# Optimization experiments

Hardware: AMD Instinct MI355X
Metric: run time of the kernel (lower is better)

The kernel has to match this reference:

```python
import jax, jax.numpy as jnp
import numpy as np

D_MODEL = 1024
N_HEAD = 16
D_HEAD = D_MODEL // N_HEAD


def setup_inputs() -> dict:
    key = jax.random.key(0)
    k_x, k_qkv, k_proj = jax.random.split(key, 3)
    B, T = 2, 2048
    x = jax.random.normal(k_x, (B, T, D_MODEL), dtype=jnp.float32)
    # torch Linear weight [out, in]; y = x @ W.T. Scale ~ kaiming-uniform-ish.
    s = 1.0 / np.sqrt(D_MODEL)
    W_qkv = jax.random.uniform(k_qkv, (3 * D_MODEL, D_MODEL), dtype=jnp.float32, minval=-s, maxval=s)
    W_proj = jax.random.uniform(k_proj, (D_MODEL, D_MODEL), dtype=jnp.float32, minval=-s, maxval=s)
    return {"x": x, "W_qkv": W_qkv, "W_proj": W_proj}


def reference(x, W_qkv, W_proj):
    B, T, C = x.shape
    qkv = jnp.einsum('btc,oc->bto', x, W_qkv)  # [B,T,3C]
    q, k, v = jnp.split(qkv, 3, axis=-1)
    # [B,T,C] -> [B,H,T,Dh]
    def heads(t):
        return t.reshape(B, T, N_HEAD, D_HEAD).transpose(0, 2, 1, 3)
    q, k, v = heads(q), heads(k), heads(v)
    scale = 1.0 / np.sqrt(D_HEAD)
    scores = jnp.einsum('bhqd,bhkd->bhqk', q, k) * scale  # [B,H,T,T]
    causal = jnp.tril(jnp.ones((T, T), dtype=bool))
    scores = jnp.where(causal, scores, jnp.finfo(scores.dtype).min)
    attn = jax.nn.softmax(scores, axis=-1)
    y = jnp.einsum('bhqk,bhkd->bhqd', attn, v)  # [B,H,T,Dh]
    y = y.transpose(0, 2, 1, 3).reshape(B, T, C)
    return jnp.einsum('btc,oc->bto', y, W_proj)
```

## Files before the change

kernel.cpp:

```cpp
#include <hip/hip_runtime.h>

typedef unsigned short u16;
typedef float f32x4 __attribute__((ext_vector_type(4)));
typedef __bf16 bf16x8 __attribute__((ext_vector_type(8)));
typedef unsigned int u32x4 __attribute__((ext_vector_type(4)));
typedef u16 u16x4 __attribute__((ext_vector_type(4)));
typedef u16 u16x8 __attribute__((ext_vector_type(8)));

static __device__ __forceinline__ u16 f2bf(float f) {
  union { __bf16 h; u16 u; } c;
  c.h = (__bf16)f;
  return c.u;
}

static __device__ __forceinline__ void gload_lds16(const void* g, void* l) {
  __builtin_amdgcn_global_load_lds(
      (const __attribute__((address_space(1))) unsigned int*)g,
      (__attribute__((address_space(3))) unsigned int*)l, 16, 0, 0);
}

__global__ __launch_bounds__(256) void cvt3_f32_bf16(const float* __restrict__ a,
                                                     const float* __restrict__ bb,
                                                     const float* __restrict__ cc,
                                                     u16* __restrict__ out,
                                                     int n1, int n2, int n3) {
  int i = blockIdx.x * 256 + threadIdx.x;
  const float* src;
  int j = i;
  if (i < n1) { src = a; }
  else if (i < n1 + n2) { src = bb; j = i - n1; }
  else { src = cc; j = i - n1 - n2; if (j >= n3) return; }
  f32x4 v = *((const f32x4*)src + j);
  u16x4 o;
  o[0] = f2bf(v[0]); o[1] = f2bf(v[1]); o[2] = f2bf(v[2]); o[3] = f2bf(v[3]);
  *((u16x4*)out + i) = o;
}

template<int OUT_BF16>
__global__ __launch_bounds__(256) void gemm_nt(const u16* __restrict__ A,
                                               const u16* __restrict__ B,
                                               void* __restrict__ Cp,
                                               int M, int N, int K, int gy) {
  __shared__ __align__(16) u16 lA[128 * 64];
  __shared__ __align__(16) u16 lB[128 * 64];
  const int tid = threadIdx.x;
  const int lane = tid & 63;
  const int wave = tid >> 6;
  const int wm = wave >> 1, wn = wave & 1;
  const int l15 = lane & 15, lg = lane >> 4;

  const int bid = blockIdx.x;
  const int xcd = bid & 7, s = bid >> 3;
  const int pnx = (N >> 7) >> 3;
  const int bm = (s % gy) * 128;
  const int bn = (xcd * pnx + s / gy) * 128;

  f32x4 acc[4][4];
#pragma unroll
  for (int i = 0; i < 4; ++i)
#pragma unroll
    for (int j = 0; j < 4; ++j) acc[i][j] = (f32x4){0.f, 0.f, 0.f, 0.f};

  const u16* Ag[4];
  const u16* Bg[4];
#pragma unroll
  for (int it = 0; it < 4; ++it) {
    const int ss = it * 256 + tid;
    const int row = ss >> 3, g = ss & 7;
    const int gsw = g ^ (row & 7);
    Ag[it] = A + (size_t)(bm + row) * K + gsw * 8;
    Bg[it] = B + (size_t)(bn + row) * K + gsw * 8;
  }

  for (int k0 = 0; k0 < K; k0 += 64) {
#pragma unroll
    for (int it = 0; it < 4; ++it) {
      gload_lds16(Ag[it] + k0, (u16*)lA + (size_t)(it * 256 + tid) * 8);
      gload_lds16(Bg[it] + k0, (u16*)lB + (size_t)(it * 256 + tid) * 8);
    }
    __syncthreads();
#pragma unroll
    for (int kk = 0; kk < 2; ++kk) {
      bf16x8 af[4], bfv[4];
#pragma unroll
      for (int mf = 0; mf < 4; ++mf) {
        const int row = wm * 64 + mf * 16 + l15;
        af[mf] = *(const bf16x8*)((const char*)lA + row * 128 +
                                  ((kk * 64 + lg * 16) ^ ((row & 7) << 4)));
      }
#pragma unroll
      for (int nf = 0; nf < 4; ++nf) {
        const int row = wn * 64 + nf * 16 + l15;
        bfv[nf] = *(const bf16x8*)((const char*)lB + row * 128 +
                                   ((kk * 64 + lg * 16) ^ ((row & 7) << 4)));
      }
#pragma unroll
      for (int mf = 0; mf < 4; ++mf)
#pragma unroll
        for (int nf = 0; nf < 4; ++nf)
          acc[mf][nf] = __builtin_amdgcn_mfma_f32_16x16x32_bf16(af[mf], bfv[nf], acc[mf][nf], 0, 0, 0);
    }
    __syncthreads();
  }

#pragma unroll
  for (int mf = 0; mf < 4; ++mf) {
#pragma unroll
    for (int r = 0; r < 4; ++r) {
      const int row = bm + wm * 64 + mf * 16 + lg * 4 + r;
#pragma unroll
      for (int nf = 0; nf < 4; ++nf) {
        const int col = bn + wn * 64 + nf * 16 + l15;
        const float v = acc[mf][nf][r];
        if (OUT_BF16) ((u16*)Cp)[(size_t)row * N + col] = f2bf(v);
        else          ((float*)Cp)[(size_t)row * N + col] = v;
      }
    }
  }
}

__global__ __launch_bounds__(256) void transpose_v(const u16* __restrict__ qkv,
                                                   u16* __restrict__ vt) {
  constexpr int T = 2048, C3 = 3072, D = 64;
  __shared__ u16 lt[64 * 65];
  const int t0 = blockIdx.x * 64;
  const int bh = blockIdx.y;
  const int b = bh >> 4, h = bh & 15;
  const int tid = threadIdx.x;
#pragma unroll
  for (int it = 0; it < 2; ++it) {
    const int c = tid + it * 256;
    const int tr = c >> 3, d0 = (c & 7) * 8;
    u32x4 v = *(const u32x4*)&qkv[((size_t)b * T + t0 + tr) * C3 + 2048 + h * D + d0];
    const u16* pv = (const u16*)&v;
#pragma unroll
    for (int e = 0; e < 8; ++e) lt[tr * 65 + d0 + e] = pv[e];
  }
  __syncthreads();
#pragma unroll
  for (int it = 0; it < 2; ++it) {
    const int c = tid + it * 256;
    const int d = c >> 3, toff = (c & 7) * 8;
    u16x8 tmp;
#pragma unroll
    for (int e = 0; e < 8; ++e) tmp[e] = lt[(toff + e) * 65 + d];
    *(u16x8*)&vt[((size_t)bh * D + d) * T + t0 + toff] = tmp;
  }
}

__global__ __launch_bounds__(256) void attn_fwd(const u16* __restrict__ qkv,
                                                const u16* __restrict__ vt,
                                                u16* __restrict__ y) {
  constexpr int T = 2048, C = 1024, C3 = 3072, D = 64, NQ = 32;
  __shared__ __align__(16) u16 lK[2][64 * 64];
  __shared__ __align__(16) u16 lV[2][64 * 64];
  __shared__ __align__(16) u16 lP[4 * 16 * 64];
  const int tid = threadIdx.x, lane = tid & 63, w = tid >> 6;
  const int l15 = lane & 15, lg = lane >> 4;

  const int bid = blockIdx.x;
  const int xcd = bid & 7, slot = bid >> 3;
  const int bh = xcd * 4 + (slot >> 4);
  const int pi = slot & 15;
  const int b = bh >> 4, h = bh & 15;

  const int r0 = tid >> 3, off0 = (tid & 7) * 8;
  const int r1 = (tid + 256) >> 3, off1 = off0;
  const int sb0 = (off0 * 2) ^ ((r0 & 7) << 4);
  const int sb1 = (off1 * 2) ^ ((r1 & 7) << 4);
  const u16* Kbase = qkv + (size_t)b * T * C3 + C + h * D;
  const u16* Vbase = vt + (size_t)bh * D * T;

  const float qscale = 0.125f * 1.44269504088896f;

#pragma unroll 1
  for (int qi = 0; qi < 2; ++qi) {
    const int qt = (qi == 0) ? pi : (NQ - 1 - pi);
    const int q0 = qt * 64;

    const size_t qoff = ((size_t)b * T + q0 + w * 16 + l15) * C3 + h * D;
    const bf16x8 aq0 = *(const bf16x8*)&qkv[qoff + lg * 8];
    const bf16x8 aq1 = *(const bf16x8*)&qkv[qoff + 32 + lg * 8];

    float m = -1.0e30f, l = 0.f;
    f32x4 o_acc[4];
#pragma unroll
    for (int nf = 0; nf < 4; ++nf) o_acc[nf] = (f32x4){0.f, 0.f, 0.f, 0.f};

    u32x4 rk0 = *(const u32x4*)(Kbase + (size_t)r0 * C3 + off0);
    u32x4 rk1 = *(const u32x4*)(Kbase + (size_t)r1 * C3 + off1);
    u32x4 rv0 = *(const u32x4*)(Vbase + (size_t)r0 * T + off0);
    u32x4 rv1 = *(const u32x4*)(Vbase + (size_t)r1 * T + off1);
    __syncthreads();
    *(u32x4*)&lK[0][(r0 * 128 + sb0) >> 1] = rk0;
    *(u32x4*)&lK[0][(r1 * 128 + sb1) >> 1] = rk1;
    *(u32x4*)&lV[0][(r0 * 128 + sb0) >> 1] = rv0;
    *(u32x4*)&lV[0][(r1 * 128 + sb1) >> 1] = rv1;
    if (qt > 0) {
      rk0 = *(const u32x4*)(Kbase + (size_t)(64 + r0) * C3 + off0);
      rk1 = *(const u32x4*)(Kbase + (size_t)(64 + r1) * C3 + off1);
      rv0 = *(const u32x4*)(Vbase + (size_t)r0 * T + 64 + off0);
      rv1 = *(const u32x4*)(Vbase + (size_t)r1 * T + 64 + off1);
    }

    for (int kt = 0; kt <= qt; ++kt) {
      const int cur = kt & 1;
      __syncthreads();
      if (kt < qt) {
        *(u32x4*)&lK[cur ^ 1][(r0 * 128 + sb0) >> 1] = rk0;
        *(u32x4*)&lK[cur ^ 1][(r1 * 128 + sb1) >> 1] = rk1;
        *(u32x4*)&lV[cur ^ 1][(r0 * 128 + sb0) >> 1] = rv0;
        *(u32x4*)&lV[cur ^ 1][(r1 * 128 + sb1) >> 1] = rv1;
        if (kt + 1 < qt) {
          const int kn = (kt + 2) * 64;
          rk0 = *(const u32x4*)(Kbase + (size_t)(kn + r0) * C3 + off0);
          rk1 = *(const u32x4*)(Kbase + (size_t)(kn + r1) * C3 + off1);
          rv0 = *(const u32x4*)(Vbase + (size_t)r0 * T + kn + off0);
          rv1 = *(const u32x4*)(Vbase + (size_t)r1 * T + kn + off1);
        }
      }
      const u16* Kc = lK[cur];
      const u16* Vc = lV[cur];

      f32x4 s[4];
#pragma unroll
      for (int nf = 0; nf < 4; ++nf) s[nf] = (f32x4){0.f, 0.f, 0.f, 0.f};
      __builtin_amdgcn_s_setprio(1);
#pragma unroll
      for (int nf = 0; nf < 4; ++nf) {
        const int row = nf * 16 + l15;
        const int x = (row & 7) << 4;
        bf16x8 bk0 = *(const bf16x8*)&Kc[(row * 128 + ((lg * 16) ^ x)) >> 1];
        bf16x8 bk1 = *(const bf16x8*)&Kc[(row * 128 + ((64 + lg * 16) ^ x)) >> 1];
        s[nf] = __builtin_amdgcn_mfma_f32_16x16x32_bf16(bk0, aq0, s[nf], 0, 0, 0);
        s[nf] = __builtin_amdgcn_mfma_f32_16x16x32_bf16(bk1, aq1, s[nf], 0, 0, 0);
      }
      __builtin_amdgcn_s_setprio(0);

#pragma unroll
      for (int nf = 0; nf < 4; ++nf) {
#pragma unroll
        for (int r = 0; r < 4; ++r) {
          float v = s[nf][r] * qscale;
          if (kt == qt) {
            if (nf * 16 + lg * 4 + r > w * 16 + l15) v = -1.0e30f;
          }
          s[nf][r] = v;
        }
      }

      float t0a = fmaxf(fmaxf(s[0][0], s[0][1]), fmaxf(s[0][2], s[0][3]));
      float t1a = fmaxf(fmaxf(s[1][0], s[1][1]), fmaxf(s[1][2], s[1][3]));
      float t2a = fmaxf(fmaxf(s[2][0], s[2][1]), fmaxf(s[2][2], s[2][3]));
      float t3a = fmaxf(fmaxf(s[3][0], s[3][1]), fmaxf(s[3][2], s[3][3]));
      float pmax = fmaxf(fmaxf(t0a, t1a), fmaxf(t2a, t3a));
      pmax = fmaxf(pmax, __shfl_xor(pmax, 16));
      pmax = fmaxf(pmax, __shfl_xor(pmax, 32));

      if (!__all(pmax <= m)) {
        const float mnew = fmaxf(m, pmax);
        const float fct = __builtin_amdgcn_exp2f(m - mnew);
        m = mnew;
        l *= fct;
#pragma unroll
        for (int r = 0; r < 4; ++r) {
          const float fr = __shfl(fct, lg * 4 + r);
#pragma unroll
          for (int nf = 0; nf < 4; ++nf) o_acc[nf][r] *= fr;
        }
      }

      float p[4][4];
#pragma unroll
      for (int nf = 0; nf < 4; ++nf)
#pragma unroll
        for (int r = 0; r < 4; ++r) p[nf][r] = __builtin_amdgcn_exp2f(s[nf][r] - m);
      float s0a = (p[0][0] + p[0][1]) + (p[0][2] + p[0][3]);
      float s1a = (p[1][0] + p[1][1]) + (p[1][2] + p[1][3]);
      float s2a = (p[2][0] + p[2][1]) + (p[2][2] + p[2][3]);
      float s3a = (p[3][0] + p[3][1]) + (p[3][2] + p[3][3]);
      float psum = (s0a + s1a) + (s2a + s3a);
      psum += __shfl_xor(psum, 16);
      psum += __shfl_xor(psum, 32);
      l += psum;

#pragma unroll
      for (int nf = 0; nf < 4; ++nf) {
        u16x4 pk;
        pk[0] = f2bf(p[nf][0]); pk[1] = f2bf(p[nf][1]);
        pk[2] = f2bf(p[nf][2]); pk[3] = f2bf(p[nf][3]);
        *(u16x4*)&lP[(w * 2048 + l15 * 128 + ((nf * 32 + lg * 8) ^ ((l15 & 7) << 4))) >> 1] = pk;
      }

      __builtin_amdgcn_s_setprio(1);
#pragma unroll
      for (int sj = 0; sj < 2; ++sj) {
        bf16x8 ap = *(const bf16x8*)&lP[(w * 2048 + l15 * 128 + ((sj * 64 + lg * 16) ^ ((l15 & 7) << 4))) >> 1];
#pragma unroll
        for (int nf = 0; nf < 4; ++nf) {
          const int d = nf * 16 + l15;
          bf16x8 bv = *(const bf16x8*)&Vc[(d * 128 + ((sj * 64 + lg * 16) ^ ((d & 7) << 4))) >> 1];
          o_acc[nf] = __builtin_amdgcn_mfma_f32_16x16x32_bf16(ap, bv, o_acc[nf], 0, 0, 0);
        }
      }
      __builtin_amdgcn_s_setprio(0);
    }

#pragma unroll
    for (int r = 0; r < 4; ++r) {
      const float li = __builtin_amdgcn_rcpf(__shfl(l, lg * 4 + r));
      const int row = q0 + w * 16 + lg * 4 + r;
#pragma unroll
      for (int nf = 0; nf < 4; ++nf) {
        const int col = h * D + nf * 16 + l15;
        y[((size_t)b * T + row) * C + col] = f2bf(o_acc[nf][r] * li);
      }
    }
  }
}

extern "C" void kernel_launch(void* const* d_in, const int* in_sizes, int n_in,
                              void* d_out, int out_size, void* d_ws, size_t ws_size,
                              hipStream_t stream) {
  const float* x = (const float*)d_in[0];
  const float* Wqkv = (const float*)d_in[1];
  const float* Wproj = (const float*)d_in[2];
  float* out = (float*)d_out;

  constexpr int B = 2, T = 2048, C = 1024, C3 = 3072, H = 16, D = 64;
  constexpr int M = B * T;

  u16* xb = (u16*)d_ws;
  u16* wqkvb = xb + (size_t)M * C;
  u16* wprojb = wqkvb + (size_t)C3 * C;
  u16* qkvb = wprojb + (size_t)C * C;
  u16* vtb = qkvb + (size_t)M * C3;
  u16* yb = vtb + (size_t)M * C;

  constexpr int n1 = (M * C) / 4, n2 = (C3 * C) / 4, n3 = (C * C) / 4;
  cvt3_f32_bf16<<<dim3((n1 + n2 + n3 + 255) / 256), 256, 0, stream>>>(
      x, Wqkv, Wproj, xb, n1, n2, n3);

  gemm_nt<1><<<dim3((C3 / 128) * (M / 128)), 256, 0, stream>>>(xb, wqkvb, qkvb, M, C3, C, M / 128);
  transpose_v<<<dim3(T / 64, B * H), 256, 0, stream>>>(qkvb, vtb);
  attn_fwd<<<dim3(512), 256, 0, stream>>>(qkvb, vtb, yb);
  gemm_nt<0><<<dim3((C / 128) * (M / 128)), 256, 0, stream>>>(yb, wprojb, out, M, C, C, M / 128);
}
```

Measured before the change: 115.4 us.

## Fuse V transpose into QKV GEMM epilogue and software-pipeline attention PV

The QKV GEMM epilogue now writes the V columns directly in transposed [b,h,d,t] layout, which removes the separate transpose_v kernel launch and its extra read and write of V. The attention loop is also skewed: QK^T for tile i is issued alongside the PV MFMA for tile i-1, using a triple-buffered V LDS buffer. This lets softmax work overlap with matrix-core work, at the cost of more LDS, an extra loop iteration and more complex control flow.

```diff
diff --git a/kernel.cpp b/kernel.cpp
--- a/kernel.cpp
+++ b/kernel.cpp
@@ -36,10 +36,11 @@
   *((u16x4*)out + i) = o;
 }
 
-template<int OUT_BF16>
+template<int OUT_BF16, int FUSE_VT>
 __global__ __launch_bounds__(256) void gemm_nt(const u16* __restrict__ A,
                                                const u16* __restrict__ B,
                                                void* __restrict__ Cp,
+                                               u16* __restrict__ vt,
                                                int M, int N, int K, int gy) {
   __shared__ __align__(16) u16 lA[128 * 64];
   __shared__ __align__(16) u16 lB[128 * 64];
@@ -103,48 +104,36 @@
     __syncthreads();
   }
 
-#pragma unroll
-  for (int mf = 0; mf < 4; ++mf) {
-#pragma unroll
-    for (int r = 0; r < 4; ++r) {
-      const int row = bm + wm * 64 + mf * 16 + lg * 4 + r;
+  if (FUSE_VT && bn >= 2048) {
+#pragma unroll
+    for (int mf = 0; mf < 4; ++mf) {
+      const int row0 = bm + wm * 64 + mf * 16 + lg * 4;
+      const int b = row0 >> 11, t0 = row0 & 2047;
 #pragma unroll
       for (int nf = 0; nf < 4; ++nf) {
-        const int col = bn + wn * 64 + nf * 16 + l15;
-        const float v = acc[mf][nf][r];
-        if (OUT_BF16) ((u16*)Cp)[(size_t)row * N + col] = f2bf(v);
-        else          ((float*)Cp)[(size_t)row * N + col] = v;
-      }
-    }
-  }
-}
-
-__global__ __launch_bounds__(256) void transpose_v(const u16* __restrict__ qkv,
-                                                   u16* __restrict__ vt) {
-  constexpr int T = 2048, C3 = 3072, D = 64;
-  __shared__ u16 lt[64 * 65];
-  const int t0 = blockIdx.x * 64;
-  const int bh = blockIdx.y;
-  const int b = bh >> 4, h = bh & 15;
-  const int tid = threadIdx.x;
-#pragma unroll
-  for (int it = 0; it < 2; ++it) {
-    const int c = tid + it * 256;
-    const int tr = c >> 3, d0 = (c & 7) * 8;
-    u32x4 v = *(const u32x4*)&qkv[((size_t)b * T + t0 + tr) * C3 + 2048 + h * D + d0];
-    const u16* pv = (const u16*)&v;
-#pragma unroll
-    for (int e = 0; e < 8; ++e) lt[tr * 65 + d0 + e] = pv[e];
-  }
-  __syncthreads();
-#pragma unroll
-  for (int it = 0; it < 2; ++it) {
-    const int c = tid + it * 256;
-    const int d = c >> 3, toff = (c & 7) * 8;
-    u16x8 tmp;
-#pragma unroll
-    for (int e = 0; e < 8; ++e) tmp[e] = lt[(toff + e) * 65 + d];
-    *(u16x8*)&vt[((size_t)bh * D + d) * T + t0 + toff] = tmp;
+        const int colv = bn - 2048 + wn * 64 + nf * 16 + l15;
+        const int h = colv >> 6, d = colv & 63;
+        u16x4 pk;
+        pk[0] = f2bf(acc[mf][nf][0]); pk[1] = f2bf(acc[mf][nf][1]);
+        pk[2] = f2bf(acc[mf][nf][2]); pk[3] = f2bf(acc[mf][nf][3]);
+        *(u16x4*)&vt[((size_t)((b * 16 + h) * 64 + d)) * 2048 + t0] = pk;
+      }
+    }
+  } else {
+#pragma unroll
+    for (int mf = 0; mf < 4; ++mf) {
+#pragma unroll
+      for (int r = 0; r < 4; ++r) {
+        const int row = bm + wm * 64 + mf * 16 + lg * 4 + r;
+#pragma unroll
+        for (int nf = 0; nf < 4; ++nf) {
+          const int col = bn + wn * 64 + nf * 16 + l15;
+          const float v = acc[mf][nf][r];
+          if (OUT_BF16) ((u16*)Cp)[(size_t)row * N + col] = f2bf(v);
+          else          ((float*)Cp)[(size_t)row * N + col] = v;
+        }
+      }
+    }
   }
 }
 
@@ -153,7 +142,7 @@
                                                 u16* __restrict__ y) {
   constexpr int T = 2048, C = 1024, C3 = 3072, D = 64, NQ = 32;
   __shared__ __align__(16) u16 lK[2][64 * 64];
-  __shared__ __align__(16) u16 lV[2][64 * 64];
+  __shared__ __align__(16) u16 lV[3][64 * 64];
   __shared__ __align__(16) u16 lP[4 * 16 * 64];
   const int tid = threadIdx.x, lane = tid & 63, w = tid >> 6;
   const int l15 = lane & 15, lg = lane >> 4;
@@ -165,9 +154,9 @@
   const int b = bh >> 4, h = bh & 15;
 
   const int r0 = tid >> 3, off0 = (tid & 7) * 8;
-  const int r1 = (tid + 256) >> 3, off1 = off0;
+  const int r1 = (tid + 256) >> 3;
   const int sb0 = (off0 * 2) ^ ((r0 & 7) << 4);
-  const int sb1 = (off1 * 2) ^ ((r1 & 7) << 4);
+  const int sb1 = (off0 * 2) ^ ((r1 & 7) << 4);
   const u16* Kbase = qkv + (size_t)b * T * C3 + C + h * D;
   const u16* Vbase = vt + (size_t)bh * D * T;
 
@@ -188,122 +177,133 @@
     for (int nf = 0; nf < 4; ++nf) o_acc[nf] = (f32x4){0.f, 0.f, 0.f, 0.f};
 
     u32x4 rk0 = *(const u32x4*)(Kbase + (size_t)r0 * C3 + off0);
-    u32x4 rk1 = *(const u32x4*)(Kbase + (size_t)r1 * C3 + off1);
+    u32x4 rk1 = *(const u32x4*)(Kbase + (size_t)r1 * C3 + off0);
     u32x4 rv0 = *(const u32x4*)(Vbase + (size_t)r0 * T + off0);
-    u32x4 rv1 = *(const u32x4*)(Vbase + (size_t)r1 * T + off1);
+    u32x4 rv1 = *(const u32x4*)(Vbase + (size_t)r1 * T + off0);
     __syncthreads();
     *(u32x4*)&lK[0][(r0 * 128 + sb0) >> 1] = rk0;
     *(u32x4*)&lK[0][(r1 * 128 + sb1) >> 1] = rk1;
     *(u32x4*)&lV[0][(r0 * 128 + sb0) >> 1] = rv0;
     *(u32x4*)&lV[0][(r1 * 128 + sb1) >> 1] = rv1;
-    if (qt > 0) {
+    if (qt >= 1) {
       rk0 = *(const u32x4*)(Kbase + (size_t)(64 + r0) * C3 + off0);
-      rk1 = *(const u32x4*)(Kbase + (size_t)(64 + r1) * C3 + off1);
+      rk1 = *(const u32x4*)(Kbase + (size_t)(64 + r1) * C3 + off0);
       rv0 = *(const u32x4*)(Vbase + (size_t)r0 * T + 64 + off0);
-      rv1 = *(const u32x4*)(Vbase + (size_t)r1 * T + 64 + off1);
-    }
-
-    for (int kt = 0; kt <= qt; ++kt) {
-      const int cur = kt & 1;
+      rv1 = *(const u32x4*)(Vbase + (size_t)r1 * T + 64 + off0);
+    }
+
+    int vcur = 0;
+    for (int i = 0; i <= qt + 1; ++i) {
+      const int vnext = (vcur == 2) ? 0 : vcur + 1;
+      const int vprev = (vcur == 0) ? 2 : vcur - 1;
       __syncthreads();
-      if (kt < qt) {
-        *(u32x4*)&lK[cur ^ 1][(r0 * 128 + sb0) >> 1] = rk0;
-        *(u32x4*)&lK[cur ^ 1][(r1 * 128 + sb1) >> 1] = rk1;
-        *(u32x4*)&lV[cur ^ 1][(r0 * 128 + sb0) >> 1] = rv0;
-        *(u32x4*)&lV[cur ^ 1][(r1 * 128 + sb1) >> 1] = rv1;
-        if (kt + 1 < qt) {
-          const int kn = (kt + 2) * 64;
+      const int wr = i + 1;
+      if (wr <= qt) {
+        *(u32x4*)&lK[wr & 1][(r0 * 128 + sb0) >> 1] = rk0;
+        *(u32x4*)&lK[wr & 1][(r1 * 128 + sb1) >> 1] = rk1;
+        *(u32x4*)&lV[vnext][(r0 * 128 + sb0) >> 1] = rv0;
+        *(u32x4*)&lV[vnext][(r1 * 128 + sb1) >> 1] = rv1;
+        if (wr + 1 <= qt) {
+          const int kn = (wr + 1) * 64;
           rk0 = *(const u32x4*)(Kbase + (size_t)(kn + r0) * C3 + off0);
-          rk1 = *(const u32x4*)(Kbase + (size_t)(kn + r1) * C3 + off1);
+          rk1 = *(const u32x4*)(Kbase + (size_t)(kn + r1) * C3 + off0);
           rv0 = *(const u32x4*)(Vbase + (size_t)r0 * T + kn + off0);
-          rv1 = *(const u32x4*)(Vbase + (size_t)r1 * T + kn + off1);
-        }
-      }
-      const u16* Kc = lK[cur];
-      const u16* Vc = lV[cur];
+          rv1 = *(const u32x4*)(Vbase + (size_t)r1 * T + kn + off0);
+        }
+      }
 
       f32x4 s[4];
-#pragma unroll
-      for (int nf = 0; nf < 4; ++nf) s[nf] = (f32x4){0.f, 0.f, 0.f, 0.f};
-      __builtin_amdgcn_s_setprio(1);
-#pragma unroll
-      for (int nf = 0; nf < 4; ++nf) {
-        const int row = nf * 16 + l15;
-        const int x = (row & 7) << 4;
-        bf16x8 bk0 = *(const bf16x8*)&Kc[(row * 128 + ((lg * 16) ^ x)) >> 1];
-        bf16x8 bk1 = *(const bf16x8*)&Kc[(row * 128 + ((64 + lg * 16) ^ x)) >> 1];
-        s[nf] = __builtin_amdgcn_mfma_f32_16x16x32_bf16(bk0, aq0, s[nf], 0, 0, 0);
-        s[nf] = __builtin_amdgcn_mfma_f32_16x16x32_bf16(bk1, aq1, s[nf], 0, 0, 0);
-      }
-      __builtin_amdgcn_s_setprio(0);
-
-#pragma unroll
-      for (int nf = 0; nf < 4; ++nf) {
-#pragma unroll
-        for (int r = 0; r < 4; ++r) {
-          float v = s[nf][r] * qscale;
-          if (kt == qt) {
-            if (nf * 16 + lg * 4 + r > w * 16 + l15) v = -1.0e30f;
+      if (i <= qt) {
+        const u16* Kc = lK[i & 1];
+#pragma unroll
+        for (int nf = 0; nf < 4; ++nf) s[nf] = (f32x4){0.f, 0.f, 0.f, 0.f};
+        __builtin_amdgcn_s_setprio(1);
+#pragma unroll
+        for (int nf = 0; nf < 4; ++nf) {
+          const int row = nf * 16 + l15;
+          const int x = (row & 7) << 4;
+          bf16x8 bk0 = *(const bf16x8*)&Kc[(row * 128 + ((lg * 16) ^ x)) >> 1];
+          bf16x8 bk1 = *(const bf16x8*)&Kc[(row * 128 + ((64 + lg * 16) ^ x)) >> 1];
+          s[nf] = __builtin_amdgcn_mfma_f32_16x16x32_bf16(bk0, aq0, s[nf], 0, 0, 0);
+          s[nf] = __builtin_amdgcn_mfma_f32_16x16x32_bf16(bk1, aq1, s[nf], 0, 0, 0);
+        }
+        __builtin_amdgcn_s_setprio(0);
+      }
+
+      if (i >= 1) {
+        const u16* Vc = lV[vprev];
+        __builtin_amdgcn_s_setprio(1);
+#pragma unroll
+        for (int sj = 0; sj < 2; ++sj) {
+          bf16x8 ap = *(const bf16x8*)&lP[(w * 2048 + l15 * 128 + ((sj * 64 + lg * 16) ^ ((l15 & 7) << 4))) >> 1];
+#pragma unroll
+          for (int nf = 0; nf < 4; ++nf) {
+            const int d = nf * 16 + l15;
+            bf16x8 bv = *(const bf16x8*)&Vc[(d * 128 + ((sj * 64 + lg * 16) ^ ((d & 7) << 4))) >> 1];
+            o_acc[nf] = __builtin_amdgcn_mfma_f32_16x16x32_bf16(ap, bv, o_acc[nf], 0, 0, 0);
           }
-          s[nf][r] = v;
-        }
-      }
-
-      float t0a = fmaxf(fmaxf(s[0][0], s[0][1]), fmaxf(s[0][2], s[0][3]));
-      float t1a = fmaxf(fmaxf(s[1][0], s[1][1]), fmaxf(s[1][2], s[1][3]));
-      float t2a = fmaxf(fmaxf(s[2][0], s[2][1]), fmaxf(s[2][2], s[2][3]));
-      float t3a = fmaxf(fmaxf(s[3][0], s[3][1]), fmaxf(s[3][2], s[3][3]));
-      float pmax = fmaxf(fmaxf(t0a, t1a), fmaxf(t2a, t3a));
-      pmax = fmaxf(pmax, __shfl_xor(pmax, 16));
-      pmax = fmaxf(pmax, __shfl_xor(pmax, 32));
-
-      if (!__all(pmax <= m)) {
-        const float mnew = fmaxf(m, pmax);
-        const float fct = __builtin_amdgcn_exp2f(m - mnew);
-        m = mnew;
-        l *= fct;
-#pragma unroll
-        for (int r = 0; r < 4; ++r) {
-          const float fr = __shfl(fct, lg * 4 + r);
-#pragma unroll
-          for (int nf = 0; nf < 4; ++nf) o_acc[nf][r] *= fr;
-        }
-      }
-
-      float p[4][4];
-#pragma unroll
-      for (int nf = 0; nf < 4; ++nf)
-#pragma unroll
-        for (int r = 0; r < 4; ++r) p[nf][r] = __builtin_amdgcn_exp2f(s[nf][r] - m);
-      float s0a = (p[0][0] + p[0][1]) + (p[0][2] + p[0][3]);
-      float s1a = (p[1][0] + p[1][1]) + (p[1][2] + p[1][3]);
-      float s2a = (p[2][0] + p[2][1]) + (p[2][2] + p[2][3]);
-      float s3a = (p[3][0] + p[3][1]) + (p[3][2] + p[3][3]);
-      float psum = (s0a + s1a) + (s2a + s3a);
-      psum += __shfl_xor(psum, 16);
-      psum += __shfl_xor(psum, 32);
-      l += psum;
-
-#pragma unroll
-      for (int nf = 0; nf < 4; ++nf) {
-        u16x4 pk;
-        pk[0] = f2bf(p[nf][0]); pk[1] = f2bf(p[nf][1]);
-        pk[2] = f2bf(p[nf][2]); pk[3] = f2bf(p[nf][3]);
-        *(u16x4*)&lP[(w * 2048 + l15 * 128 + ((nf * 32 + lg * 8) ^ ((l15 & 7) << 4))) >> 1] = pk;
-      }
-
-      __builtin_amdgcn_s_setprio(1);
-#pragma unroll
-      for (int sj = 0; sj < 2; ++sj) {
-        bf16x8 ap = *(const bf16x8*)&lP[(w * 2048 + l15 * 128 + ((sj * 64 + lg * 16) ^ ((l15 & 7) << 4))) >> 1];
+        }
+        __builtin_amdgcn_s_setprio(0);
+      }
+
+      if (i <= qt) {
 #pragma unroll
         for (int nf = 0; nf < 4; ++nf) {
-          const int d = nf * 16 + l15;
-          bf16x8 bv = *(const bf16x8*)&Vc[(d * 128 + ((sj * 64 + lg * 16) ^ ((d & 7) << 4))) >> 1];
-          o_acc[nf] = __builtin_amdgcn_mfma_f32_16x16x32_bf16(ap, bv, o_acc[nf], 0, 0, 0);
-        }
-      }
-      __builtin_amdgcn_s_setprio(0);
+#pragma unroll
+          for (int r = 0; r < 4; ++r) {
+            float v = s[nf][r] * qscale;
+            if (i == qt) {
+              if (nf * 16 + lg * 4 + r > w * 16 + l15) v = -1.0e30f;
+            }
+            s[nf][r] = v;
+          }
+        }
+
+        float t0a = fmaxf(fmaxf(s[0][0], s[0][1]), fmaxf(s[0][2], s[0][3]));
+        float t1a = fmaxf(fmaxf(s[1][0], s[1][1]), fmaxf(s[1][2], s[1][3]));
+        float t2a = fmaxf(fmaxf(s[2][0], s[2][1]), fmaxf(s[2][2], s[2][3]));
+        float t3a = fmaxf(fmaxf(s[3][0], s[3][1]), fmaxf(s[3][2], s[3][3]));
+        float pmax = fmaxf(fmaxf(t0a, t1a), fmaxf(t2a, t3a));
+        pmax = fmaxf(pmax, __shfl_xor(pmax, 16));
+        pmax = fmaxf(pmax, __shfl_xor(pmax, 32));
+
+        if (!__all(pmax <= m)) {
+          const float mnew = fmaxf(m, pmax);
+          const float fct = __builtin_amdgcn_exp2f(m - mnew);
+          m = mnew;
+          l *= fct;
+#pragma unroll
+          for (int r = 0; r < 4; ++r) {
+            const float fr = __shfl(fct, lg * 4 + r);
+#pragma unroll
+            for (int nf = 0; nf < 4; ++nf) o_acc[nf][r] *= fr;
+          }
+        }
+
+        float p[4][4];
+#pragma unroll
+        for (int nf = 0; nf < 4; ++nf)
+#pragma unroll
+          for (int r = 0; r < 4; ++r) p[nf][r] = __builtin_amdgcn_exp2f(s[nf][r] - m);
+        float s0a = (p[0][0] + p[0][1]) + (p[0][2] + p[0][3]);
+        float s1a = (p[1][0] + p[1][1]) + (p[1][2] + p[1][3]);
+        float s2a = (p[2][0] + p[2][1]) + (p[2][2] + p[2][3]);
+        float s3a = (p[3][0] + p[3][1]) + (p[3][2] + p[3][3]);
+        float psum = (s0a + s1a) + (s2a + s3a);
+        psum += __shfl_xor(psum, 16);
+        psum += __shfl_xor(psum, 32);
+        l += psum;
+
+#pragma unroll
+        for (int nf = 0; nf < 4; ++nf) {
+          u16x4 pk;
+          pk[0] = f2bf(p[nf][0]); pk[1] = f2bf(p[nf][1]);
+          pk[2] = f2bf(p[nf][2]); pk[3] = f2bf(p[nf][3]);
+          *(u16x4*)&lP[(w * 2048 + l15 * 128 + ((nf * 32 + lg * 8) ^ ((l15 & 7) << 4))) >> 1] = pk;
+        }
+      }
+
+      vcur = vnext;
     }
 
 #pragma unroll
@@ -341,8 +341,9 @@
   cvt3_f32_bf16<<<dim3((n1 + n2 + n3 + 255) / 256), 256, 0, stream>>>(
       x, Wqkv, Wproj, xb, n1, n2, n3);
 
-  gemm_nt<1><<<dim3((C3 / 128) * (M / 128)), 256, 0, stream>>>(xb, wqkvb, qkvb, M, C3, C, M / 128);
-  transpose_v<<<dim3(T / 64, B * H), 256, 0, stream>>>(qkvb, vtb);
+  gemm_nt<1, 1><<<dim3((C3 / 128) * (M / 128)), 256, 0, stream>>>(
+      xb, wqkvb, qkvb, vtb, M, C3, C, M / 128);
   attn_fwd<<<dim3(512), 256, 0, stream>>>(qkvb, vtb, yb);
-  gemm_nt<0><<<dim3((C / 128) * (M / 128)), 256, 0, stream>>>(yb, wprojb, out, M, C, C, M / 128);
-}
+  gemm_nt<0, 0><<<dim3((C / 128) * (M / 128)), 256, 0, stream>>>(
+      yb, wprojb, out, nullptr, M, C, C, M / 128);
+}
```

Result: no change. 114.5 us (-0.8%).
